# Performance work log

Measured on AMD Instinct MI355X. Metric: run time of the kernel, lower is better.

## Reference

```python
import jax, jax.numpy as jnp
import numpy as np


def setup_inputs() -> dict:
    key = jax.random.key(0)
    k1, k2 = jax.random.split(key)
    B, L, D = 8, 2048, 256
    x = jax.random.normal(k1, (B, L, D), dtype=jnp.float32)
    x_mask = jax.random.randint(k2, (B, L), 0, 2).astype(bool)  # True = padded key position
    return {"x": x, "x_mask": x_mask}


def reference(x, x_mask):
    # x: [B, L, D], x_mask: [B, L] bool (True = masked/padding)
    B, L, D = x.shape
    # Unscaled self-attention scores: [B, L, L]
    scores = jnp.einsum('bld,bmd->blm', x, x)
    # Diagonal exclusion: score of token with itself set to 0 (not -inf!)
    eye = jnp.eye(L, dtype=bool)
    scores = jnp.where(eye[None, :, :], jnp.float32(0.0), scores)
    # Padding mask: mask key columns with -inf (applied after diagonal zeroing,
    # so a masked diagonal entry ends up -inf, matching the torch order of ops)
    scores = jnp.where(x_mask[:, None, :], -jnp.inf, scores)
    a = jax.nn.softmax(scores, axis=2)
    return jnp.einsum('blm,bmd->bld', a, x)
```

## Files before the change

### kernel.cpp

```cpp
#include <hip/hip_runtime.h>
#include <hip/hip_bf16.h>

#define B_ 8
#define L_ 2048
#define D_ 256
#define BK 32
#define KSPLIT 2
#define KQ (L_/KSPLIT)
#define NIT (KQ/BK)
#define PSTR 40
#define NROW (B_*L_)
#define NE ((size_t)B_*L_*D_)
#define THR 6.0f
#define MINIT (-1e30f)

typedef __attribute__((ext_vector_type(8))) _Float16 f16x8;
typedef __attribute__((ext_vector_type(4))) _Float16 hf4;
typedef __attribute__((ext_vector_type(4))) float f32x4;

#define MFMA16F(a,b,c) __builtin_amdgcn_mfma_f32_16x16x32_f16((a),(b),(c),0,0,0)
#define NEG_INF (-__builtin_inff())
#define GLL(src,dst) __builtin_amdgcn_global_load_lds( \
    (const __attribute__((address_space(1))) void*)(src), \
    (__attribute__((address_space(3))) void*)(dst), 16, 0, 0)

__device__ __forceinline__ f32x4 fmax4(f32x4 a, f32x4 b){
  f32x4 r;
  r[0]=fmaxf(a[0],b[0]); r[1]=fmaxf(a[1],b[1]);
  r[2]=fmaxf(a[2],b[2]); r[3]=fmaxf(a[3],b[3]);
  return r;
}

__global__ void prep_k(const float* __restrict__ x,
                       _Float16* __restrict__ x16,
                       _Float16* __restrict__ vtl){
  __shared__ _Float16 T[64][258];
  const int t = threadIdx.x;
  const int l0 = blockIdx.x*64, b = blockIdx.y;
  const int r = t>>5, c = (t&31)*8;
  #pragma unroll
  for (int p=0;p<8;++p){
    int row = r + p*8;
    size_t idx = ((size_t)(b*L_ + l0 + row))*D_ + c;
    float4 v0 = *(const float4*)(x + idx);
    float4 v1 = *(const float4*)(x + idx + 4);
    f16x8 h;
    h[0]=(_Float16)v0.x; h[1]=(_Float16)v0.y; h[2]=(_Float16)v0.z; h[3]=(_Float16)v0.w;
    h[4]=(_Float16)v1.x; h[5]=(_Float16)v1.y; h[6]=(_Float16)v1.z; h[7]=(_Float16)v1.w;
    *(f16x8*)(x16 + idx) = h;
    #pragma unroll
    for (int j=0;j<8;++j) T[row][c+j] = h[j];
  }
  __syncthreads();
  _Float16* vb = vtl + ((size_t)(b*64 + blockIdx.x*2))*8192;
  #pragma unroll
  for (int i=0;i<8;++i){
    int n = t + 256*i;
    int q = n & 1023, tile = n>>10;
    int d = q>>2, ph = q&3;
    int kc = ph ^ ((d>>1)&3);
    int k0 = tile*32 + kc*8;
    f16x8 h;
    #pragma unroll
    for (int j=0;j<8;++j) h[j] = T[k0+j][d];
    *(f16x8*)(vb + (size_t)n*8) = h;
  }
}

__launch_bounds__(256, 2)
__global__ void flash_k(const _Float16* __restrict__ x16,
                        const _Float16* __restrict__ vtl,
                        const int* __restrict__ mask,
                        _Float16* __restrict__ oall,
                        float* __restrict__ mll,
                        float* __restrict__ mm){
  __shared__ __attribute__((aligned(16))) _Float16 sK[2][8192];
  __shared__ __attribute__((aligned(16))) _Float16 sV[2][8192];
  __shared__ __attribute__((aligned(16))) _Float16 sP[2][4][16*PSTR];

  const int tid  = threadIdx.x;
  const int wave = tid >> 6, lane = tid & 63;
  const int quad = lane >> 4, l16 = lane & 15;
  const int b = blockIdx.y, z = blockIdx.z;
  const int q0w = blockIdx.x*64 + wave*16;
  const int sw = l16 & 7, vsw = (l16>>1)&3;

  f16x8 qh[8];
  {
    const _Float16* qr = x16 + ((size_t)(b*L_ + q0w + l16))*D_;
    #pragma unroll
    for (int ks=0; ks<8; ++ks)
      qh[ks] = *(const f16x8*)(qr + ks*32 + quad*8);
  }
  unsigned long long mb = 0;
  {
    const int* mrow = mask + b*L_ + z*KQ;
    #pragma unroll
    for (int j=0;j<64;++j)
      mb |= (unsigned long long)(mrow[j*16 + l16] ? 1u : 0u) << j;
  }

  f32x4 M = (f32x4){MINIT, MINIT, MINIT, MINIT};

  unsigned kof[4], vof[4], dof[4];
  #pragma unroll
  for (int i=0;i<4;++i){
    int c = (wave + i*4)*64 + lane;
    int r = c>>5, pk = c&31;
    kof[i] = (unsigned)(r*512 + ((pk ^ (r&7))*16));
    vof[i] = (unsigned)(c*16);
    dof[i] = (unsigned)((wave + i*4)*1024);
  }
  const char* kbase = (const char*)x16 + ((size_t)b*L_ + (size_t)z*KQ)*(D_*2);
  const char* vbase = (const char*)vtl + ((size_t)(b*64 + z*32))*16384;

  #pragma unroll
  for (int i=0;i<4;++i) GLL(kbase + kof[i], (char*)sK[0] + dof[i]);

  f32x4 O[16], Osum;
  #pragma unroll
  for (int i=0;i<16;i++) O[i] = (f32x4){0.f,0.f,0.f,0.f};
  Osum = (f32x4){0.f,0.f,0.f,0.f};
  f16x8 ones;
  #pragma unroll
  for (int j=0;j<8;++j) ones[j] = (_Float16)1.0f;

  __syncthreads();

  for (int it=0; it<NIT; ++it){
    if (it+1 < NIT){
      const char* kb2 = kbase + (size_t)(it+1)*16384;
      char* kd = (char*)sK[(it+1)&1];
      #pragma unroll
      for (int i=0;i<4;++i) GLL(kb2 + kof[i], kd + dof[i]);
    }
    {
      const char* vb2 = vbase + (size_t)it*16384;
      char* vd = (char*)sV[it&1];
      #pragma unroll
      for (int i=0;i<4;++i) GLL(vb2 + vof[i], vd + dof[i]);
    }
    const _Float16* kb = sK[it&1];

    f32x4 S[2];
    S[0]=(f32x4){0,0,0,0}; S[1]=(f32x4){0,0,0,0};
    #pragma unroll
    for (int ks=0; ks<8; ++ks){
      f16x8 b0 = *(const f16x8*)(kb + (     l16)*256 + (((ks*4+quad)^sw)*8));
      f16x8 b1 = *(const f16x8*)(kb + (16 + l16)*256 + (((ks*4+quad)^sw)*8));
      S[0] = MFMA16F(qh[ks], b0, S[0]);
      S[1] = MFMA16F(qh[ks], b1, S[1]);
    }

    if (it > 0){
      const _Float16* vb = sV[(it-1)&1];
      f16x8 pf = *(const f16x8*)(&sP[(it-1)&1][wave][l16*PSTR + quad*8]);
      #pragma unroll
      for (int vt=0; vt<16; ++vt){
        f16x8 bv = *(const f16x8*)(vb + (vt*16+l16)*32 + ((quad^vsw)*8));
        O[vt] = MFMA16F(pf, bv, O[vt]);
      }
      Osum = MFMA16F(pf, ones, Osum);
    }

    {
      const int d0 = q0w - (z*KQ + it*BK);
      if ((unsigned)d0 < 32u){
        const int ntd = d0 >> 4;
        #pragma unroll
        for (int r=0;r<4;++r)
          S[ntd][r] = (l16 == quad*4+r) ? 0.0f : S[ntd][r];
      }
    }
    {
      const unsigned mw = (unsigned)(mb >> (unsigned)(it*2));
      const float mk0 = (mw & 1u) ? NEG_INF : 0.0f;
      const float mk1 = (mw & 2u) ? NEG_INF : 0.0f;
      #pragma unroll
      for (int r=0;r<4;++r){ S[0][r] += mk0; S[1][r] += mk1; }
    }

    {
      f32x4 t = fmax4(S[0], S[1]);
      int ok = 1;
      #pragma unroll
      for (int r=0;r<4;++r) ok &= (t[r] <= M[r] + THR);
      if (!__all(ok)){
        #pragma unroll
        for (int off=1; off<16; off<<=1){
          f32x4 o;
          o[0]=__shfl_xor(t[0],off); o[1]=__shfl_xor(t[1],off);
          o[2]=__shfl_xor(t[2],off); o[3]=__shfl_xor(t[3],off);
          t = fmax4(t,o);
        }
        f32x4 mn = fmax4(M, t);
        float sc[4];
        #pragma unroll
        for (int r=0;r<4;++r) sc[r] = __expf(M[r] - mn[r]);
        #pragma unroll
        for (int vt=0; vt<16; ++vt){
          #pragma unroll
          for (int r=0;r<4;++r) O[vt][r] *= sc[r];
        }
        #pragma unroll
        for (int r=0;r<4;++r) Osum[r] *= sc[r];
        M = mn;
      }
    }

    #pragma unroll
    for (int r=0;r<4;++r){
      const int row = quad*4 + r;
      sP[it&1][wave][row*PSTR +      l16] = (_Float16)__expf(S[0][r] - M[r]);
      sP[it&1][wave][row*PSTR + 16 + l16] = (_Float16)__expf(S[1][r] - M[r]);
    }

    __syncthreads();
  }

  {
    const _Float16* vb = sV[(NIT-1)&1];
    f16x8 pf = *(const f16x8*)(&sP[(NIT-1)&1][wave][l16*PSTR + quad*8]);
    #pragma unroll
    for (int vt=0; vt<16; ++vt){
      f16x8 bv = *(const f16x8*)(vb + (vt*16+l16)*32 + ((quad^vsw)*8));
      O[vt] = MFMA16F(pf, bv, O[vt]);
    }
    Osum = MFMA16F(pf, ones, Osum);
  }

  {
    const int u = b*(L_/16) + blockIdx.x*4 + wave;
    _Float16* ob = oall + (size_t)z*NE + (size_t)u*4096;
    #pragma unroll
    for (int vt=0; vt<16; ++vt){
      hf4 hh;
      #pragma unroll
      for (int r=0;r<4;++r) hh[r] = (_Float16)O[vt][r];
      *(hf4*)(ob + vt*256 + lane*4) = hh;
    }
    if (l16 == 0){
      const int row = u*16 + quad*4;
      #pragma unroll
      for (int r=0;r<4;++r){
        mll[z*NROW + row + r] = Osum[r];
        mm [z*NROW + row + r] = M[r];
      }
    }
  }
}

__global__ void combine_k(float* __restrict__ out,
                          const _Float16* __restrict__ oall,
                          const float* __restrict__ mll,
                          const float* __restrict__ mm){
  __shared__ float T2[16][260];
  const int t = threadIdx.x, u = blockIdx.x;
  const int quad = (t>>4)&3, l16 = t&15;
  const int row0 = u*16 + quad*4;

  f32x4 mz[KSPLIT], lz[KSPLIT];
  #pragma unroll
  for (int zc=0; zc<KSPLIT; ++zc){
    mz[zc] = *(const f32x4*)(mm  + zc*NROW + row0);
    lz[zc] = *(const f32x4*)(mll + zc*NROW + row0);
  }
  f32x4 ms = mz[0];
  #pragma unroll
  for (int zc=1; zc<KSPLIT; ++zc) ms = fmax4(ms, mz[zc]);

  float sc[KSPLIT][4];
  f32x4 den = (f32x4){0.f,0.f,0.f,0.f};
  #pragma unroll
  for (int zc=0; zc<KSPLIT; ++zc){
    #pragma unroll
    for (int r=0;r<4;++r){
      sc[zc][r] = __expf(mz[zc][r] - ms[r]);
      den[r] += sc[zc][r] * lz[zc][r];
    }
  }
  float inv[4];
  #pragma unroll
  for (int r=0;r<4;++r) inv[r] = 1.0f/den[r];

  #pragma unroll
  for (int i=0;i<4;++i){
    const int f = t + 256*i;
    const int vt = f>>6;
    float acc[4] = {0.f,0.f,0.f,0.f};
    #pragma unroll
    for (int zc=0; zc<KSPLIT; ++zc){
      hf4 v = *(const hf4*)(oall + (size_t)zc*NE + (size_t)u*4096 + (size_t)f*4);
      #pragma unroll
      for (int r=0;r<4;++r) acc[r] += sc[zc][r] * (float)v[r];
    }
    #pragma unroll
    for (int r=0;r<4;++r) T2[quad*4+r][vt*16+l16] = acc[r]*inv[r];
  }
  __syncthreads();
  #pragma unroll
  for (int p=0;p<4;++p){
    const int row = (t>>6) + p*4, col = (t&63)*4;
    float4 vv = *(const float4*)&T2[row][col];
    *(float4*)(out + ((size_t)u*16 + row)*D_ + col) = vv;
  }
}

extern "C" void kernel_launch(void* const* d_in, const int* in_sizes, int n_in,
                              void* d_out, int out_size, void* d_ws, size_t ws_size,
                              hipStream_t stream) {
  const float* x    = (const float*)d_in[0];
  const int*   mask = (const int*)d_in[1];
  float*       out  = (float*)d_out;

  _Float16* x16  = (_Float16*)d_ws;
  _Float16* vtl  = x16 + NE;
  _Float16* oall = vtl + NE;
  float*    mll  = (float*)(oall + (size_t)KSPLIT*NE);
  float*    mm   = mll + (size_t)KSPLIT*NROW;

  prep_k   <<<dim3(L_/64, B_), dim3(256), 0, stream>>>(x, x16, vtl);
  flash_k  <<<dim3(L_/64, B_, KSPLIT), dim3(256), 0, stream>>>(x16, vtl, mask, oall, mll, mm);
  combine_k<<<dim3(NROW/16), dim3(256), 0, stream>>>(out, oall, mll, mm);
}
```

Before: 145.7 us.

## Fold log2e into Q, use exp2, raise rescale threshold, shrink prep tiles

```diff
diff --git a/kernel.cpp b/kernel.cpp
--- a/kernel.cpp
+++ b/kernel.cpp
@@ -11,8 +11,9 @@
 #define PSTR 40
 #define NROW (B_*L_)
 #define NE ((size_t)B_*L_*D_)
-#define THR 6.0f
+#define THR 13.0f
 #define MINIT (-1e30f)
+#define LOG2E_F 1.44269504f
 
 typedef __attribute__((ext_vector_type(8))) _Float16 f16x8;
 typedef __attribute__((ext_vector_type(4))) _Float16 hf4;
@@ -34,13 +35,17 @@
 __global__ void prep_k(const float* __restrict__ x,
                        _Float16* __restrict__ x16,
                        _Float16* __restrict__ vtl){
-  __shared__ _Float16 T[64][258];
+  __shared__ _Float16 T[32][258];
   const int t = threadIdx.x;
-  const int l0 = blockIdx.x*64, b = blockIdx.y;
-  const int r = t>>5, c = (t&31)*8;
-  #pragma unroll
-  for (int p=0;p<8;++p){
-    int row = r + p*8;
+  const int tIdx = blockIdx.x;
+  const int b = blockIdx.y;
+  const int l0 = tIdx*32;
+
+  #pragma unroll
+  for (int i=0;i<4;++i){
+    const int n8 = t + 256*i;
+    const int row = n8>>5;
+    const int c   = (n8&31)*8;
     size_t idx = ((size_t)(b*L_ + l0 + row))*D_ + c;
     float4 v0 = *(const float4*)(x + idx);
     float4 v1 = *(const float4*)(x + idx + 4);
@@ -48,22 +53,21 @@
     h[0]=(_Float16)v0.x; h[1]=(_Float16)v0.y; h[2]=(_Float16)v0.z; h[3]=(_Float16)v0.w;
     h[4]=(_Float16)v1.x; h[5]=(_Float16)v1.y; h[6]=(_Float16)v1.z; h[7]=(_Float16)v1.w;
     *(f16x8*)(x16 + idx) = h;
-    #pragma unroll
-    for (int j=0;j<8;++j) T[row][c+j] = h[j];
+    *(f16x8*)(&T[row][c]) = h;
   }
   __syncthreads();
-  _Float16* vb = vtl + ((size_t)(b*64 + blockIdx.x*2))*8192;
-  #pragma unroll
-  for (int i=0;i<8;++i){
-    int n = t + 256*i;
-    int q = n & 1023, tile = n>>10;
-    int d = q>>2, ph = q&3;
-    int kc = ph ^ ((d>>1)&3);
-    int k0 = tile*32 + kc*8;
+
+  _Float16* vb = vtl + ((size_t)(b*64 + tIdx))*8192;
+  #pragma unroll
+  for (int i=0;i<4;++i){
+    const int q = t + 256*i;
+    const int d = q>>2, ph = q&3;
+    const int kc = ph ^ ((d>>1)&3);
+    const int k0 = kc*8;
     f16x8 h;
     #pragma unroll
     for (int j=0;j<8;++j) h[j] = T[k0+j][d];
-    *(f16x8*)(vb + (size_t)n*8) = h;
+    *(f16x8*)(vb + (size_t)q*8) = h;
   }
 }
 
@@ -88,9 +92,14 @@
   f16x8 qh[8];
   {
     const _Float16* qr = x16 + ((size_t)(b*L_ + q0w + l16))*D_;
-    #pragma unroll
-    for (int ks=0; ks<8; ++ks)
-      qh[ks] = *(const f16x8*)(qr + ks*32 + quad*8);
+    const _Float16 l2e = (_Float16)LOG2E_F;
+    #pragma unroll
+    for (int ks=0; ks<8; ++ks){
+      f16x8 h = *(const f16x8*)(qr + ks*32 + quad*8);
+      #pragma unroll
+      for (int j=0;j<8;++j) h[j] = h[j] * l2e;
+      qh[ks] = h;
+    }
   }
   unsigned long long mb = 0;
   {
@@ -196,7 +205,7 @@
         f32x4 mn = fmax4(M, t);
         float sc[4];
         #pragma unroll
-        for (int r=0;r<4;++r) sc[r] = __expf(M[r] - mn[r]);
+        for (int r=0;r<4;++r) sc[r] = exp2f(M[r] - mn[r]);
         #pragma unroll
         for (int vt=0; vt<16; ++vt){
           #pragma unroll
@@ -211,8 +220,8 @@
     #pragma unroll
     for (int r=0;r<4;++r){
       const int row = quad*4 + r;
-      sP[it&1][wave][row*PSTR +      l16] = (_Float16)__expf(S[0][r] - M[r]);
-      sP[it&1][wave][row*PSTR + 16 + l16] = (_Float16)__expf(S[1][r] - M[r]);
+      sP[it&1][wave][row*PSTR +      l16] = (_Float16)exp2f(S[0][r] - M[r]);
+      sP[it&1][wave][row*PSTR + 16 + l16] = (_Float16)exp2f(S[1][r] - M[r]);
     }
 
     __syncthreads();
@@ -275,7 +284,7 @@
   for (int zc=0; zc<KSPLIT; ++zc){
     #pragma unroll
     for (int r=0;r<4;++r){
-      sc[zc][r] = __expf(mz[zc][r] - ms[r]);
+      sc[zc][r] = exp2f(mz[zc][r] - ms[r]);
       den[r] += sc[zc][r] * lz[zc][r];
     }
   }
@@ -319,7 +328,7 @@
   float*    mll  = (float*)(oall + (size_t)KSPLIT*NE);
   float*    mm   = mll + (size_t)KSPLIT*NROW;
 
-  prep_k   <<<dim3(L_/64, B_), dim3(256), 0, stream>>>(x, x16, vtl);
+  prep_k   <<<dim3(L_/32, B_), dim3(256), 0, stream>>>(x, x16, vtl);
   flash_k  <<<dim3(L_/64, B_, KSPLIT), dim3(256), 0, stream>>>(x16, vtl, mask, oall, mll, mm);
   combine_k<<<dim3(NROW/16), dim3(256), 0, stream>>>(out, oall, mll, mm);
 }
```

Measured after the change: 148.4 us. About the same (+1.9%).
